# Optimization experiments

Hardware: AMD Instinct MI355X
Metric: run time of the kernel (lower is better)

Reference implementation:

```python
import jax, jax.numpy as jnp
import numpy as np

N, E, D_IN, D_HID, D_OUT = 50000, 800000, 128, 128, 64

def setup_inputs() -> dict:
    key = jax.random.key(0)
    ks = jax.random.split(key, 20)
    inp = {
        'x': jax.random.normal(ks[0], (N, D_IN), dtype=jnp.float32),
        'edge_index': jax.random.randint(ks[1], (2, E), 0, N, dtype=jnp.int64),
        'edge_attr': jax.random.normal(ks[2], (E, 16), dtype=jnp.float32),
        'edge_weight': jax.random.uniform(ks[3], (E,), dtype=jnp.float32),
    }
    dims = [(D_IN, D_HID), (D_HID, D_HID), (D_HID, D_OUT)]
    for i, (di, do) in enumerate(dims):
        s = 1.0 / np.sqrt(di)
        inp[f'Wl{i}'] = jax.random.uniform(ks[4 + 5 * i], (di, do), minval=-s, maxval=s, dtype=jnp.float32)
        inp[f'bl{i}'] = jnp.zeros((do,), dtype=jnp.float32)
        inp[f'Wr{i}'] = jax.random.uniform(ks[5 + 5 * i], (di, do), minval=-s, maxval=s, dtype=jnp.float32)
        inp[f'Ws{i}'] = jax.random.uniform(ks[6 + 5 * i], (di, do), minval=-s, maxval=s, dtype=jnp.float32)
        inp[f'bs{i}'] = jnp.zeros((do,), dtype=jnp.float32)
    return inp


def _sage(x, src, dst, Wl, bl, Wr):
    # mean aggregation of source features at target nodes (PyG SAGEConv)
    msg = x[src]                                               # [E, d] gather
    ssum = jax.ops.segment_sum(msg, dst, num_segments=N)        # [N, d]
    cnt = jax.ops.segment_sum(jnp.ones((src.shape[0],), x.dtype), dst, num_segments=N)
    agg = ssum / jnp.maximum(cnt, 1.0)[:, None]
    return agg @ Wl + bl + x @ Wr                               # lin_l(agg) + lin_r(x)


def reference(x, edge_index, edge_attr, edge_weight,
              Wl0, bl0, Wr0, Ws0, bs0,
              Wl1, bl1, Wr1, Ws1, bs1,
              Wl2, bl2, Wr2, Ws2, bs2):
    src, dst = edge_index[0], edge_index[1]
    h = jax.nn.relu(_sage(x, src, dst, Wl0, bl0, Wr0) + x @ Ws0 + bs0)
    h = jax.nn.relu(_sage(h, src, dst, Wl1, bl1, Wr1) + h @ Ws1 + bs1)
    out = _sage(h, src, dst, Wl2, bl2, Wr2) + h @ Ws2 + bs2
    return out
```

## Files before the change

kernel.cpp:

```cpp
#include <hip/hip_runtime.h>
#include <hip/hip_bf16.h>


#define LB __launch_bounds__

typedef __attribute__((ext_vector_type(8))) short short8;
typedef __attribute__((ext_vector_type(4))) float f32x4;

__device__ __forceinline__ unsigned short bf16_rne(float f) {
  unsigned u = __builtin_bit_cast(unsigned, f);
  unsigned r = u + 0x7fffu + ((u >> 16) & 1u);
  return (unsigned short)(r >> 16);
}
__device__ __forceinline__ float bf16_to_f(unsigned short us) {
  return __builtin_bit_cast(float, (unsigned)us << 16);
}
__device__ __forceinline__ float bits_to_f(unsigned u) {
  return __builtin_bit_cast(float, u);
}

__device__ __forceinline__ void async16(const void* g, void* l) {
  __builtin_amdgcn_global_load_lds((const __attribute__((address_space(1))) unsigned*)g,
                                   (__attribute__((address_space(3))) unsigned*)l, 16, 0, 0);
}

#define BCAP 8192
#define P1_CHUNK 4096

__device__ __forceinline__ void p1_body(int bid, const int* __restrict__ src,
                                        const int* __restrict__ dst, int* __restrict__ bcnt,
                                        int2* __restrict__ pairs, int E) {
  __shared__ int cnt[256];
  __shared__ int base[256];
  const int tid = threadIdx.x;
  cnt[tid] = 0;
  __syncthreads();
  const int e0 = bid * P1_CHUNK;
  int myb[16], myr[16], mys[16], myd[16];
#pragma unroll
  for (int i = 0; i < 16; ++i) {
    int e = e0 + i * 256 + tid;
    myb[i] = -1;
    if (e < E) {
      int s = src[e], d = dst[e];
      int b = d >> 8;
      myb[i] = b;
      mys[i] = s;
      myd[i] = d;
      myr[i] = atomicAdd(&cnt[b], 1);
    }
  }
  __syncthreads();
  base[tid] = (cnt[tid] > 0) ? atomicAdd(&bcnt[tid], cnt[tid]) : 0;
  __syncthreads();
#pragma unroll
  for (int i = 0; i < 16; ++i) {
    int b = myb[i];
    if (b >= 0) {
      int p = base[b] + myr[i];
      if (p < BCAP) pairs[(size_t)b * BCAP + p] = make_int2(mys[i], myd[i]);
    }
  }
}

__device__ __forceinline__ void p234_body(int b, const int2* __restrict__ pairs,
                                          const int* __restrict__ bcnt, int* __restrict__ gcounter,
                                          int* __restrict__ row_start, int* __restrict__ deg_arr,
                                          float* __restrict__ scale, int* __restrict__ srcs, int N) {
  __shared__ int h[256];
  __shared__ int sc[256];
  __shared__ int cur[256];
  __shared__ int shared_bb;
  const int tid = threadIdx.x;
  h[tid] = 0;
  __syncthreads();
  int m = bcnt[b];
  if (m > BCAP) m = BCAP;
  for (int i = tid; i < m; i += 256) {
    atomicAdd(&h[pairs[(size_t)b * BCAP + i].y & 255], 1);
  }
  __syncthreads();
  const int deg = h[tid];
  sc[tid] = deg;
  __syncthreads();
  for (int off = 1; off < 256; off <<= 1) {
    int add = (tid >= off) ? sc[tid - off] : 0;
    __syncthreads();
    sc[tid] += add;
    __syncthreads();
  }
  if (tid == 0) shared_bb = atomicAdd(gcounter, sc[255]);
  __syncthreads();
  const int abs_off = shared_bb + sc[tid] - deg;
  const int node = b * 256 + tid;
  if (node < N) {
    row_start[node] = abs_off;
    deg_arr[node] = deg;
    scale[node] = 1.0f / (float)(deg > 1 ? deg : 1);
  }
  cur[tid] = abs_off;
  __syncthreads();
  for (int i = tid; i < m; i += 256) {
    int2 pr = pairs[(size_t)b * BCAP + i];
    int p = atomicAdd(&cur[pr.y & 255], 1);
    srcs[p] = pr.x;
  }
}

__device__ __forceinline__ void wpack_body(int wb, const float* __restrict__ Wl0,
                                           const float* __restrict__ Wr0,
                                           const float* __restrict__ Ws0,
                                           const float* __restrict__ bl0,
                                           const float* __restrict__ bs0,
                                           const float* __restrict__ Wl1,
                                           const float* __restrict__ Wr1,
                                           const float* __restrict__ Ws1,
                                           const float* __restrict__ bl1,
                                           const float* __restrict__ bs1,
                                           const float* __restrict__ Wl2,
                                           const float* __restrict__ Wr2,
                                           const float* __restrict__ Ws2,
                                           const float* __restrict__ bl2,
                                           const float* __restrict__ bs2, ushort* __restrict__ Bh0,
                                           ushort* __restrict__ Bo0, float* __restrict__ bb0,
                                           ushort* __restrict__ Bh1, ushort* __restrict__ Bo1,
                                           float* __restrict__ bb1, ushort* __restrict__ Bh2,
                                           ushort* __restrict__ Bo2, float* __restrict__ bb2) {
  const int layer = wb >> 7;
  const int xb = wb & 127;
  const float *Wl, *Wr, *Ws, *bl, *bs;
  ushort *Bh, *Bo;
  float* bb;
  int M;
  if (layer == 0) {
    Wl = Wl0; Wr = Wr0; Ws = Ws0; bl = bl0; bs = bs0; Bh = Bh0; Bo = Bo0; bb = bb0; M = 256;
  } else if (layer == 1) {
    Wl = Wl1; Wr = Wr1; Ws = Ws1; bl = bl1; bs = bs1; Bh = Bh1; Bo = Bo1; bb = bb1; M = 256;
  } else {
    Wl = Wl2; Wr = Wr2; Ws = Ws2; bl = bl2; bs = bs2; Bh = Bh2; Bo = Bo2; bb = bb2; M = 128;
  }
  const int DO = M / 2;
  int idx = xb * 256 + (int)threadIdx.x;
  if (idx < 128 * M) {
    int k = idx / M, c = idx - k * M;
    float v = (c < DO) ? Wl[k * DO + c] : (Wr[k * DO + (c - DO)] + Ws[k * DO + (c - DO)]);
    unsigned short h = bf16_rne(v);
    unsigned short l = bf16_rne(v - bf16_to_f(h));
    int d = ((k >> 3) * M + c) * 8 + (k & 7);
    Bh[d] = h;
    Bo[d] = l;
  }
  if (idx < DO) bb[idx] = bl[idx] + bs[idx];
}

__device__ __forceinline__ void split8v(f32x4 f0, f32x4 f1, short8& h, short8& l) {
  float f[8] = {f0[0], f0[1], f0[2], f0[3], f1[0], f1[1], f1[2], f1[3]};
#pragma unroll
  for (int j = 0; j < 8; ++j) {
    unsigned u = __builtin_bit_cast(unsigned, f[j]);
    h[j] = (short)(u >> 16);
    l[j] = (short)bf16_rne(f[j] - bits_to_f(u & 0xffff0000u));
  }
}

template <int M>
__device__ __forceinline__ void gemm_compute(int bx, const char* smem,
                                             const ushort* __restrict__ Bhi,
                                             const ushort* __restrict__ Blo,
                                             ushort* __restrict__ Yb, float* __restrict__ Z,
                                             int n) {
  constexpr int DO = M / 2;
  constexpr int NWC = (M >= 256) ? 4 : 2;
  constexpr int NWR = 4 / NWC;
  constexpr int BROWS = 32 * NWR;
  const int tid = threadIdx.x;
  const int w = tid >> 6, l = tid & 63;
  const int q = l >> 4, m16 = l & 15;
  const int rowBase = bx * BROWS + (w / NWC) * 32;
  const int colBase = (w % NWC) * 64;

  f32x4 acc[2][4] = {};
  const int rl0 = (w / NWC) * 32 + m16;

#pragma unroll
  for (int s = 0; s < 4; ++s) {
    short8 ah[2], al[2], bh[4], bo[4];
    const int kb = s * 4 + q;
#pragma unroll
    for (int i = 0; i < 2; ++i) {
      int rl = rl0 + i * 16;
      int g0 = (2 * kb) ^ m16;
      int g1 = (2 * kb + 1) ^ m16;
      f32x4 fa = *(const f32x4*)(smem + (size_t)rl * 512 + g0 * 16);
      f32x4 fb = *(const f32x4*)(smem + (size_t)rl * 512 + g1 * 16);
      split8v(fa, fb, ah[i], al[i]);
    }
#pragma unroll
    for (int j = 0; j < 4; ++j) {
      size_t off = ((size_t)kb * M + colBase + j * 16 + m16) * 8;
      bh[j] = *(const short8*)(Bhi + off);
      bo[j] = *(const short8*)(Blo + off);
    }
#pragma unroll
    for (int i = 0; i < 2; ++i)
#pragma unroll
      for (int j = 0; j < 4; ++j) {
        acc[i][j] = __builtin_amdgcn_mfma_f32_16x16x32_bf16(ah[i], bh[j], acc[i][j], 0, 0, 0);
        acc[i][j] = __builtin_amdgcn_mfma_f32_16x16x32_bf16(ah[i], bo[j], acc[i][j], 0, 0, 0);
        acc[i][j] = __builtin_amdgcn_mfma_f32_16x16x32_bf16(al[i], bh[j], acc[i][j], 0, 0, 0);
      }
  }

#pragma unroll
  for (int i = 0; i < 2; ++i) {
    int rb = rowBase + i * 16 + q * 4;
#pragma unroll
    for (int j = 0; j < 4; ++j) {
      int c = colBase + j * 16 + m16;
#pragma unroll
      for (int r = 0; r < 4; ++r) {
        int row = rb + r;
        if (row < n) {
          float v = acc[i][j][r];
          if (c < DO)
            Yb[(size_t)row * DO + c] = bf16_rne(v);
          else
            Z[(size_t)row * DO + (c - DO)] = v;
        }
      }
    }
  }
}

__device__ __forceinline__ void gemm0_body(int bx, const float* __restrict__ x,
                                           const ushort* __restrict__ Bh,
                                           const ushort* __restrict__ Bo, ushort* __restrict__ Yb,
                                           float* __restrict__ Z, int n, char* smem) {
  const int tid = threadIdx.x;
  const int wbase = tid & ~63;
#pragma unroll
  for (int r = 0; r < 4; ++r) {
    int ell = r * 256 + tid;
    int row = ell >> 5, gl = ell & 31;
    int grow = bx * 32 + row;
    if (grow >= n) grow = n - 1;
    int gs = gl ^ (row & 15);
    async16(x + (size_t)grow * 128 + gs * 4, smem + (size_t)(r * 256 + wbase) * 16);
  }
  __syncthreads();
  gemm_compute<256>(bx, smem, Bh, Bo, Yb, Z, n);
}

__device__ __forceinline__ void acc8(float* a, uint4 u) {
  a[0] += bits_to_f(u.x << 16);
  a[1] += bits_to_f(u.x & 0xffff0000u);
  a[2] += bits_to_f(u.y << 16);
  a[3] += bits_to_f(u.y & 0xffff0000u);
  a[4] += bits_to_f(u.z << 16);
  a[5] += bits_to_f(u.z & 0xffff0000u);
  a[6] += bits_to_f(u.w << 16);
  a[7] += bits_to_f(u.w & 0xffff0000u);
}

template <int M>
__global__ LB(256, 3) void fused_agg_gemm(const ushort* __restrict__ Y,
                                          const float* __restrict__ Zprev,
                                          const int* __restrict__ row_start,
                                          const int* __restrict__ deg_arr,
                                          const int* __restrict__ srcs,
                                          const float* __restrict__ scale,
                                          const float* __restrict__ bsum,
                                          const ushort* __restrict__ Bhi,
                                          const ushort* __restrict__ Blo, ushort* __restrict__ Yb,
                                          float* __restrict__ Zf, int n) {
  constexpr int BROWS = (M >= 256) ? 32 : 64;
  constexpr int ECAP = (M >= 256) ? 2048 : 4096;
  __shared__ __align__(16) char smem[BROWS * 512];
  __shared__ int eidx[ECAP];
  __shared__ int rs_s[BROWS];
  __shared__ int deg_s[BROWS];
  const int tid = threadIdx.x;
  const int w = tid >> 6;
  const int lane = tid & 63;
  const int qt = lane >> 4;
  const int li = lane & 15;
  const int blockRow0 = blockIdx.x * BROWS;
  const uint4* Y4 = (const uint4*)Y;

  if (tid < BROWS) {
    int node = blockRow0 + tid;
    int cn = node < n ? node : n - 1;
    rs_s[tid] = row_start[cn];
    deg_s[tid] = node < n ? deg_arr[node] : 0;
  }
  __syncthreads();
  const int lastValid = (n - blockRow0 < BROWS ? n - blockRow0 : BROWS) - 1;
  const int rs0 = rs_s[0];
  const int total = rs_s[lastValid] + deg_s[lastValid] - rs0;
  const int stage = total < ECAP ? total : ECAP;
  for (int i = tid; i < stage; i += 256) eidx[i] = srcs[rs0 + i];
  __syncthreads();

#pragma unroll 2
  for (int t = 0; t < BROWS / 4; ++t) {
    const int r = t * 4 + w;
    const int node = blockRow0 + r;
    const bool live = node < n;
    float a[8] = {0.f, 0.f, 0.f, 0.f, 0.f, 0.f, 0.f, 0.f};
    float4 z0, z1, b0, b1;
    float sc = 0.f;
    if (live) {
      const int base = rs_s[r] - rs0;
      const int cnt = deg_s[r];
      if (qt == 0) {
        sc = scale[node];
        z0 = ((const float4*)Zprev)[(size_t)node * 32 + 2 * li];
        z1 = ((const float4*)Zprev)[(size_t)node * 32 + 2 * li + 1];
        b0 = ((const float4*)bsum)[2 * li];
        b1 = ((const float4*)bsum)[2 * li + 1];
      }
      int avail = ECAP - base;
      if (avail < 0) avail = 0;
      const int cin = cnt < avail ? cnt : avail;
      int j = 0;
      for (; j + 16 <= cin; j += 16) {
        int s0 = eidx[base + j + qt];
        int s1 = eidx[base + j + 4 + qt];
        int s2 = eidx[base + j + 8 + qt];
        int s3 = eidx[base + j + 12 + qt];
        uint4 u0 = Y4[(size_t)s0 * 16 + li];
        uint4 u1 = Y4[(size_t)s1 * 16 + li];
        uint4 u2 = Y4[(size_t)s2 * 16 + li];
        uint4 u3 = Y4[(size_t)s3 * 16 + li];
        acc8(a, u0);
        acc8(a, u1);
        acc8(a, u2);
        acc8(a, u3);
      }
      for (; j + 4 <= cin; j += 4) {
        int s = eidx[base + j + qt];
        uint4 u = Y4[(size_t)s * 16 + li];
        acc8(a, u);
      }
      {
        int rem = cin - j;
        if (rem > 0) {
          int s = eidx[base + j + (qt < rem ? qt : 0)];
          if (qt < rem) {
            uint4 u = Y4[(size_t)s * 16 + li];
            acc8(a, u);
          }
        }
      }
      if (cin < cnt) {
        int e = cin;
        const int abs0 = rs_s[r];
        for (; e + 4 <= cnt; e += 4) {
          int s = srcs[abs0 + e + qt];
          uint4 u = Y4[(size_t)s * 16 + li];
          acc8(a, u);
        }
        int rem = cnt - e;
        if (rem > 0) {
          int s = srcs[abs0 + e + (qt < rem ? qt : 0)];
          if (qt < rem) {
            uint4 u = Y4[(size_t)s * 16 + li];
            acc8(a, u);
          }
        }
      }
    }
#pragma unroll
    for (int k = 0; k < 8; ++k) {
      a[k] += __shfl(a[k], lane ^ 16);
      a[k] += __shfl(a[k], lane ^ 32);
    }
    float4 o0 = make_float4(0.f, 0.f, 0.f, 0.f);
    float4 o1 = make_float4(0.f, 0.f, 0.f, 0.f);
    if (live && qt == 0) {
      o0.x = fmaxf(z0.x + sc * a[0] + b0.x, 0.f);
      o0.y = fmaxf(z0.y + sc * a[1] + b0.y, 0.f);
      o0.z = fmaxf(z0.z + sc * a[2] + b0.z, 0.f);
      o0.w = fmaxf(z0.w + sc * a[3] + b0.w, 0.f);
      o1.x = fmaxf(z1.x + sc * a[4] + b1.x, 0.f);
      o1.y = fmaxf(z1.y + sc * a[5] + b1.y, 0.f);
      o1.z = fmaxf(z1.z + sc * a[6] + b1.z, 0.f);
      o1.w = fmaxf(z1.w + sc * a[7] + b1.w, 0.f);
    }
    if (qt == 0) {
      *(float4*)(smem + (size_t)r * 512 + (size_t)(((2 * li) ^ (r & 15)) * 16)) = o0;
      *(float4*)(smem + (size_t)r * 512 + (size_t)(((2 * li + 1) ^ (r & 15)) * 16)) = o1;
    }
  }
  __syncthreads();
  gemm_compute<M>(blockIdx.x, smem, Bhi, Blo, Yb, Zf, n);
}

__global__ LB(256) void fused_wpack_p1(const int* __restrict__ src, const int* __restrict__ dst,
                                       int* __restrict__ bcnt, int2* __restrict__ pairs, int E,
                                       int NP1, const float* Wl0, const float* Wr0, const float* Ws0,
                                       const float* bl0, const float* bs0, const float* Wl1,
                                       const float* Wr1, const float* Ws1, const float* bl1,
                                       const float* bs1, const float* Wl2, const float* Wr2,
                                       const float* Ws2, const float* bl2, const float* bs2,
                                       ushort* Bh0, ushort* Bo0, float* bb0, ushort* Bh1,
                                       ushort* Bo1, float* bb1, ushort* Bh2, ushort* Bo2,
                                       float* bb2) {
  if ((int)blockIdx.x < NP1) {
    p1_body(blockIdx.x, src, dst, bcnt, pairs, E);
  } else {
    wpack_body(blockIdx.x - NP1, Wl0, Wr0, Ws0, bl0, bs0, Wl1, Wr1, Ws1, bl1, bs1, Wl2, Wr2, Ws2,
               bl2, bs2, Bh0, Bo0, bb0, Bh1, Bo1, bb1, Bh2, Bo2, bb2);
  }
}

__global__ LB(256, 3) void fused_p234_gemm0(const int2* __restrict__ pairs,
                                            const int* __restrict__ bcnt, int* __restrict__ gcounter,
                                            int* __restrict__ row_start, int* __restrict__ deg_arr,
                                            float* __restrict__ scale, int* __restrict__ srcs, int N,
                                            const float* __restrict__ x,
                                            const ushort* __restrict__ Bh0,
                                            const ushort* __restrict__ Bo0, ushort* __restrict__ Yb,
                                            float* __restrict__ Zf, int NB) {
  __shared__ __align__(16) char smem[32 * 512];
  if ((int)blockIdx.x < NB) {
    p234_body(blockIdx.x, pairs, bcnt, gcounter, row_start, deg_arr, scale, srcs, N);
  } else {
    gemm0_body(blockIdx.x - NB, x, Bh0, Bo0, Yb, Zf, N, smem);
  }
}

__global__ LB(256) void agg64_kernel(const ushort* __restrict__ Y, const float* __restrict__ Z,
                                     const int* __restrict__ row_start,
                                     const int* __restrict__ deg_arr, const int* __restrict__ srcs,
                                     const float* __restrict__ scale, const float* __restrict__ bsum,
                                     float* __restrict__ out, int n) {
  int node = blockIdx.x * 4 + (threadIdx.x >> 6);
  if (node >= n) return;
  const int lane = threadIdx.x & 63;
  const int li = lane & 15;
  const int qt = lane >> 4;
  const int e0 = row_start[node];
  const int cnt = deg_arr[node];
  const int end = e0 + cnt;
  const int c1 = cnt < 64 ? cnt : 64;
  int idx = (lane < c1) ? srcs[e0 + lane] : 0;
  const uint2* Yu = (const uint2*)Y;
  float a0 = 0.f, a1 = 0.f, a2 = 0.f, a3 = 0.f;

  int j = 0;
  for (; j + 16 <= c1; j += 16) {
    int s0 = __shfl(idx, j + qt);
    int s1 = __shfl(idx, j + 4 + qt);
    int s2 = __shfl(idx, j + 8 + qt);
    int s3 = __shfl(idx, j + 12 + qt);
    uint2 u0 = Yu[(size_t)s0 * 16 + li];
    uint2 u1 = Yu[(size_t)s1 * 16 + li];
    uint2 u2 = Yu[(size_t)s2 * 16 + li];
    uint2 u3 = Yu[(size_t)s3 * 16 + li];
    a0 += bits_to_f(u0.x << 16) + bits_to_f(u1.x << 16) + bits_to_f(u2.x << 16) +
          bits_to_f(u3.x << 16);
    a1 += bits_to_f(u0.x & 0xffff0000u) + bits_to_f(u1.x & 0xffff0000u) +
          bits_to_f(u2.x & 0xffff0000u) + bits_to_f(u3.x & 0xffff0000u);
    a2 += bits_to_f(u0.y << 16) + bits_to_f(u1.y << 16) + bits_to_f(u2.y << 16) +
          bits_to_f(u3.y << 16);
    a3 += bits_to_f(u0.y & 0xffff0000u) + bits_to_f(u1.y & 0xffff0000u) +
          bits_to_f(u2.y & 0xffff0000u) + bits_to_f(u3.y & 0xffff0000u);
  }
  for (; j + 4 <= c1; j += 4) {
    int s = __shfl(idx, j + qt);
    uint2 u = Yu[(size_t)s * 16 + li];
    a0 += bits_to_f(u.x << 16);
    a1 += bits_to_f(u.x & 0xffff0000u);
    a2 += bits_to_f(u.y << 16);
    a3 += bits_to_f(u.y & 0xffff0000u);
  }
  {
    int rem = c1 - j;
    if (rem > 0) {
      int s = __shfl(idx, j + (qt < rem ? qt : 0));
      if (qt < rem) {
        uint2 u = Yu[(size_t)s * 16 + li];
        a0 += bits_to_f(u.x << 16);
        a1 += bits_to_f(u.x & 0xffff0000u);
        a2 += bits_to_f(u.y << 16);
        a3 += bits_to_f(u.y & 0xffff0000u);
      }
    }
  }
  if (cnt > 64) {
    int e = e0 + 64;
    for (; e + 4 <= end; e += 4) {
      int s = srcs[e + qt];
      uint2 u = Yu[(size_t)s * 16 + li];
      a0 += bits_to_f(u.x << 16);
      a1 += bits_to_f(u.x & 0xffff0000u);
      a2 += bits_to_f(u.y << 16);
      a3 += bits_to_f(u.y & 0xffff0000u);
    }
    int rem = end - e;
    if (qt < rem) {
      int s = srcs[e + qt];
      uint2 u = Yu[(size_t)s * 16 + li];
      a0 += bits_to_f(u.x << 16);
      a1 += bits_to_f(u.x & 0xffff0000u);
      a2 += bits_to_f(u.y << 16);
      a3 += bits_to_f(u.y & 0xffff0000u);
    }
  }
  a0 += __shfl(a0, lane ^ 16);
  a1 += __shfl(a1, lane ^ 16);
  a2 += __shfl(a2, lane ^ 16);
  a3 += __shfl(a3, lane ^ 16);
  a0 += __shfl(a0, lane ^ 32);
  a1 += __shfl(a1, lane ^ 32);
  a2 += __shfl(a2, lane ^ 32);
  a3 += __shfl(a3, lane ^ 32);

  if (qt == 0) {
    float sc = scale[node];
    float4 z = ((const float4*)Z)[(size_t)node * 16 + li];
    float4 b = ((const float4*)bsum)[li];
    float4 o;
    o.x = z.x + sc * a0 + b.x;
    o.y = z.y + sc * a1 + b.y;
    o.z = z.z + sc * a2 + b.z;
    o.w = z.w + sc * a3 + b.w;
    ((float4*)out)[(size_t)node * 16 + li] = o;
  }
}

extern "C" void kernel_launch(void* const* d_in, const int* in_sizes, int n_in,
                              void* d_out, int out_size, void* d_ws, size_t ws_size,
                              hipStream_t stream) {
  const float* x = (const float*)d_in[0];
  const int* ei = (const int*)d_in[1];
  const int N = in_sizes[0] / 128;
  const int E = in_sizes[3];
  const int* src = ei;
  const int* dst = ei + E;
  const float* Wl[3] = {(const float*)d_in[4], (const float*)d_in[9], (const float*)d_in[14]};
  const float* bl[3] = {(const float*)d_in[5], (const float*)d_in[10], (const float*)d_in[15]};
  const float* Wr[3] = {(const float*)d_in[6], (const float*)d_in[11], (const float*)d_in[16]};
  const float* Ws[3] = {(const float*)d_in[7], (const float*)d_in[12], (const float*)d_in[17]};
  const float* bs[3] = {(const float*)d_in[8], (const float*)d_in[13], (const float*)d_in[18]};

  const int NB = (N + 255) >> 8;
  const int NP1 = (E + P1_CHUNK - 1) / P1_CHUNK;

  size_t off = 0;
  auto carve = [&](size_t bytes) -> char* {
    char* p = (char*)d_ws + off;
    off += (bytes + 255) & ~(size_t)255;
    return p;
  };
  int* row_start = (int*)carve((size_t)N * 4);
  int* deg_arr = (int*)carve((size_t)N * 4);
  int* bcnt = (int*)carve((size_t)NB * 4);
  int* gcounter = (int*)carve(256);
  float* scale = (float*)carve((size_t)N * 4);
  int* srcs = (int*)carve((size_t)E * 4);
  int2* pairs = (int2*)carve((size_t)NB * BCAP * 8);
  ushort* Yb0 = (ushort*)carve((size_t)N * 128 * 2);
  float* Zf0 = (float*)carve((size_t)N * 128 * 4);
  ushort* Yb1 = (ushort*)carve((size_t)N * 128 * 2);
  float* Zf1 = (float*)carve((size_t)N * 128 * 4);
  ushort* Bh[3];
  ushort* Bo[3];
  float* bsum[3];
  for (int i = 0; i < 3; ++i) {
    Bh[i] = (ushort*)carve(128 * 256 * 2);
    Bo[i] = (ushort*)carve(128 * 256 * 2);
    bsum[i] = (float*)carve(128 * 4);
  }
  (void)ws_size;
  (void)n_in;
  (void)out_size;

  size_t bcnt_pad = ((size_t)NB * 4 + 255) & ~(size_t)255;
  hipMemsetAsync(bcnt, 0, bcnt_pad + 4, stream);

  fused_wpack_p1<<<NP1 + 384, 256, 0, stream>>>(
      src, dst, bcnt, pairs, E, NP1, Wl[0], Wr[0], Ws[0], bl[0], bs[0], Wl[1], Wr[1], Ws[1], bl[1],
      bs[1], Wl[2], Wr[2], Ws[2], bl[2], bs[2], Bh[0], Bo[0], bsum[0], Bh[1], Bo[1], bsum[1], Bh[2],
      Bo[2], bsum[2]);

  int g32 = (N + 31) / 32;
  int g64 = (N + 63) / 64;
  int gAgg = (N + 3) / 4;

  fused_p234_gemm0<<<NB + g32, 256, 0, stream>>>(pairs, bcnt, gcounter, row_start, deg_arr, scale,
                                                 srcs, N, x, Bh[0], Bo[0], Yb0, Zf0, NB);
  fused_agg_gemm<256><<<g32, 256, 0, stream>>>(Yb0, Zf0, row_start, deg_arr, srcs, scale, bsum[0],
                                               Bh[1], Bo[1], Yb1, Zf1, N);
  fused_agg_gemm<128><<<g64, 256, 0, stream>>>(Yb1, Zf1, row_start, deg_arr, srcs, scale, bsum[1],
                                               Bh[2], Bo[2], Yb0, Zf0, N);
  agg64_kernel<<<gAgg, 256, 0, stream>>>(Yb0, Zf0, row_start, deg_arr, srcs, scale, bsum[2],
                                         (float*)d_out, N);
}
```

Measured before the change: 315.1 us.

## Replace LDS edge-index staging with per-wave register loads and shuffles

The fused aggregation+GEMM kernel no longer stages each block's source indices into a large shared-memory array behind two block barriers. Each wave now loads up to 64 neighbour indices for its node into registers and hands them out with wave shuffles, reading any extra indices directly from global memory. This frees a lot of LDS, and the launch bounds are raised so more waves can be resident to hide gather latency. In exchange the row loop is no longer unrolled, and the tighter register budget may cause spills.

```diff
diff --git a/kernel.cpp b/kernel.cpp
--- a/kernel.cpp
+++ b/kernel.cpp
@@ -263,22 +263,14 @@
 }
 
 template <int M>
-__global__ LB(256, 3) void fused_agg_gemm(const ushort* __restrict__ Y,
-                                          const float* __restrict__ Zprev,
-                                          const int* __restrict__ row_start,
-                                          const int* __restrict__ deg_arr,
-                                          const int* __restrict__ srcs,
-                                          const float* __restrict__ scale,
-                                          const float* __restrict__ bsum,
-                                          const ushort* __restrict__ Bhi,
-                                          const ushort* __restrict__ Blo, ushort* __restrict__ Yb,
-                                          float* __restrict__ Zf, int n) {
+__global__ LB(256, (M >= 256 ? 5 : 4)) void fused_agg_gemm(
+    const ushort* __restrict__ Y, const float* __restrict__ Zprev,
+    const int* __restrict__ row_start, const int* __restrict__ deg_arr,
+    const int* __restrict__ srcs, const float* __restrict__ scale,
+    const float* __restrict__ bsum, const ushort* __restrict__ Bhi,
+    const ushort* __restrict__ Blo, ushort* __restrict__ Yb, float* __restrict__ Zf, int n) {
   constexpr int BROWS = (M >= 256) ? 32 : 64;
-  constexpr int ECAP = (M >= 256) ? 2048 : 4096;
   __shared__ __align__(16) char smem[BROWS * 512];
-  __shared__ int eidx[ECAP];
-  __shared__ int rs_s[BROWS];
-  __shared__ int deg_s[BROWS];
   const int tid = threadIdx.x;
   const int w = tid >> 6;
   const int lane = tid & 63;
@@ -287,21 +279,7 @@
   const int blockRow0 = blockIdx.x * BROWS;
   const uint4* Y4 = (const uint4*)Y;
 
-  if (tid < BROWS) {
-    int node = blockRow0 + tid;
-    int cn = node < n ? node : n - 1;
-    rs_s[tid] = row_start[cn];
-    deg_s[tid] = node < n ? deg_arr[node] : 0;
-  }
-  __syncthreads();
-  const int lastValid = (n - blockRow0 < BROWS ? n - blockRow0 : BROWS) - 1;
-  const int rs0 = rs_s[0];
-  const int total = rs_s[lastValid] + deg_s[lastValid] - rs0;
-  const int stage = total < ECAP ? total : ECAP;
-  for (int i = tid; i < stage; i += 256) eidx[i] = srcs[rs0 + i];
-  __syncthreads();
-
-#pragma unroll 2
+#pragma unroll 1
   for (int t = 0; t < BROWS / 4; ++t) {
     const int r = t * 4 + w;
     const int node = blockRow0 + r;
@@ -310,8 +288,10 @@
     float4 z0, z1, b0, b1;
     float sc = 0.f;
     if (live) {
-      const int base = rs_s[r] - rs0;
-      const int cnt = deg_s[r];
+      const int e0 = row_start[node];
+      const int cnt = deg_arr[node];
+      const int c1 = cnt < 64 ? cnt : 64;
+      int idx = (lane < c1) ? srcs[e0 + lane] : 0;
       if (qt == 0) {
         sc = scale[node];
         z0 = ((const float4*)Zprev)[(size_t)node * 32 + 2 * li];
@@ -319,15 +299,12 @@
         b0 = ((const float4*)bsum)[2 * li];
         b1 = ((const float4*)bsum)[2 * li + 1];
       }
-      int avail = ECAP - base;
-      if (avail < 0) avail = 0;
-      const int cin = cnt < avail ? cnt : avail;
       int j = 0;
-      for (; j + 16 <= cin; j += 16) {
-        int s0 = eidx[base + j + qt];
-        int s1 = eidx[base + j + 4 + qt];
-        int s2 = eidx[base + j + 8 + qt];
-        int s3 = eidx[base + j + 12 + qt];
+      for (; j + 16 <= c1; j += 16) {
+        int s0 = __shfl(idx, j + qt);
+        int s1 = __shfl(idx, j + 4 + qt);
+        int s2 = __shfl(idx, j + 8 + qt);
+        int s3 = __shfl(idx, j + 12 + qt);
         uint4 u0 = Y4[(size_t)s0 * 16 + li];
         uint4 u1 = Y4[(size_t)s1 * 16 + li];
         uint4 u2 = Y4[(size_t)s2 * 16 + li];
@@ -337,36 +314,33 @@
         acc8(a, u2);
         acc8(a, u3);
       }
-      for (; j + 4 <= cin; j += 4) {
-        int s = eidx[base + j + qt];
+      for (; j + 4 <= c1; j += 4) {
+        int s = __shfl(idx, j + qt);
         uint4 u = Y4[(size_t)s * 16 + li];
         acc8(a, u);
       }
       {
-        int rem = cin - j;
+        int rem = c1 - j;
         if (rem > 0) {
-          int s = eidx[base + j + (qt < rem ? qt : 0)];
+          int s = __shfl(idx, j + (qt < rem ? qt : 0));
           if (qt < rem) {
             uint4 u = Y4[(size_t)s * 16 + li];
             acc8(a, u);
           }
         }
       }
-      if (cin < cnt) {
-        int e = cin;
-        const int abs0 = rs_s[r];
+      if (cnt > 64) {
+        int e = 64;
         for (; e + 4 <= cnt; e += 4) {
-          int s = srcs[abs0 + e + qt];
+          int s = srcs[e0 + e + qt];
           uint4 u = Y4[(size_t)s * 16 + li];
           acc8(a, u);
         }
         int rem = cnt - e;
-        if (rem > 0) {
-          int s = srcs[abs0 + e + (qt < rem ? qt : 0)];
-          if (qt < rem) {
-            uint4 u = Y4[(size_t)s * 16 + li];
-            acc8(a, u);
-          }
+        if (qt < rem) {
+          int s = srcs[e0 + e + qt];
+          uint4 u = Y4[(size_t)s * 16 + li];
+          acc8(a, u);
         }
       }
     }
@@ -414,7 +388,7 @@
   }
 }
 
-__global__ LB(256, 3) void fused_p234_gemm0(const int2* __restrict__ pairs,
+__global__ LB(256, 5) void fused_p234_gemm0(const int2* __restrict__ pairs,
                                             const int* __restrict__ bcnt, int* __restrict__ gcounter,
                                             int* __restrict__ row_start, int* __restrict__ deg_arr,
                                             float* __restrict__ scale, int* __restrict__ srcs, int N,
```

New measurement: 305.2 us. 3.1% less time.
